# Performance work log

Measured on AMD Instinct MI355X. Metric: run time of the kernel, lower is better.

The kernel has to match this reference:

```python
import jax, jax.numpy as jnp
import numpy as np

EPS = 1e-5
K = 5


def _bn(h, g, b):
    # BatchNorm1d in training mode: batch stats over all dims except channels.
    ax = tuple(range(h.ndim - 1))
    mu = jnp.mean(h, axis=ax, keepdims=True)
    var = jnp.var(h, axis=ax, keepdims=True)
    return g * (h - mu) * jax.lax.rsqrt(var + EPS) + b


def _block(x, w, b, g, be):
    # Lin -> ReLU -> BN, as in MLP() helper
    return _bn(jax.nn.relu(x @ w + b), g, be)


def _knn_idx(x, k):
    # x: [B, P, D]; k nearest per point (includes self at distance 0)
    sq = jnp.sum(x * x, axis=-1)
    d2 = sq[:, :, None] + sq[:, None, :] - 2.0 * jnp.einsum('bpd,bqd->bpq', x, x)
    return jax.lax.top_k(-d2, k)[1]  # [B, P, k]


def _edge_conv(x, k, mlp_fn):
    # DynamicEdgeConv: recompute kNN graph on current features, gather
    # neighbor/center pairs, per-edge MLP on [x_i, x_j - x_i], max-aggregate.
    idx = _knn_idx(x, k)                                   # [B,P,k]
    xj = jax.vmap(lambda xb, ib: xb[ib])(x, idx)           # [B,P,k,D]
    xi = jnp.broadcast_to(x[:, :, None, :], xj.shape)
    e = jnp.concatenate([xi, xj - xi], axis=-1)            # [B,P,k,2D]
    return jnp.max(mlp_fn(e), axis=2)                      # max aggr -> [B,P,C]


def dec_forward(pos,
                c1w0, c1b0, c1g0, c1e0,
                c1w1, c1b1, c1g1, c1e1,
                c1w2, c1b2, c1g2, c1e2,
                c2w, c2b, c2g, c2e,
                l1w, l1b, l1g, l1e,
                m1w, m1b, m1g, m1e,
                m2w, m2b, m2g, m2e,
                m3w, m3b):
    mlp1 = lambda e: _block(_block(_block(e, c1w0, c1b0, c1g0, c1e0),
                                   c1w1, c1b1, c1g1, c1e1),
                            c1w2, c1b2, c1g2, c1e2)
    x1 = _edge_conv(pos, K, mlp1)                          # [B,P,64]
    x2 = _edge_conv(x1, K, lambda e: _block(e, c2w, c2b, c2g, c2e))  # [B,P,128]
    h = _block(jnp.concatenate([x1, x2], axis=-1), l1w, l1b, l1g, l1e)  # [B,P,1024]
    p = jnp.max(h, axis=1)                                 # global_max_pool -> [B,1024]
    p = _block(p, m1w, m1b, m1g, m1e)                      # dropout omitted (eval)
    p = _block(p, m2w, m2b, m2g, m2e)
    return p @ m3w + m3b                                   # [B, n_classes]


def setup_inputs() -> dict:
    key = jax.random.key(0)
    ks = jax.random.split(key, 12)
    B, P = 16, 2048

    def w(k, shape):
        return 0.05 * jax.random.normal(k, shape, jnp.float32)

    z = lambda c: jnp.zeros((c,), jnp.float32)
    o = lambda c: jnp.ones((c,), jnp.float32)

    d = {
        'pos': jax.random.normal(ks[0], (B, P, 3), jnp.float32),
        'c1w0': w(ks[1], (6, 64)), 'c1b0': z(64), 'c1g0': o(64), 'c1e0': z(64),
        'c1w1': w(ks[2], (64, 64)), 'c1b1': z(64), 'c1g1': o(64), 'c1e1': z(64),
        'c1w2': w(ks[3], (64, 64)), 'c1b2': z(64), 'c1g2': o(64), 'c1e2': z(64),
        'c2w': w(ks[4], (128, 128)), 'c2b': z(128), 'c2g': o(128), 'c2e': z(128),
        'l1w': w(ks[5], (192, 1024)), 'l1b': z(1024), 'l1g': o(1024), 'l1e': z(1024),
        'm1w': w(ks[6], (1024, 512)), 'm1b': z(512), 'm1g': o(512), 'm1e': z(512),
        'm2w': w(ks[7], (512, 256)), 'm2b': z(256), 'm2g': o(256), 'm2e': z(256),
        'm3w': w(ks[8], (256, 2)), 'm3b': z(2),
    }
    return d


def reference(pos,
              c1w0, c1b0, c1g0, c1e0,
              c1w1, c1b1, c1g1, c1e1,
              c1w2, c1b2, c1g2, c1e2,
              c2w, c2b, c2g, c2e,
              l1w, l1b, l1g, l1e,
              m1w, m1b, m1g, m1e,
              m2w, m2b, m2g, m2e,
              m3w, m3b):
    return dec_forward(pos,
                       c1w0, c1b0, c1g0, c1e0,
                       c1w1, c1b1, c1g1, c1e1,
                       c1w2, c1b2, c1g2, c1e2,
                       c2w, c2b, c2g, c2e,
                       l1w, l1b, l1g, l1e,
                       m1w, m1b, m1g, m1e,
                       m2w, m2b, m2g, m2e,
                       m3w, m3b)
```

## Files before the change

### kernel.cpp

```cpp
#include <hip/hip_runtime.h>
#include <cmath>

constexpr int B = 16, P = 2048, KNN = 5;
constexpr int BP = B * P;
constexpr int E = BP * KNN;
constexpr float EPS = 1e-5f;
constexpr int QC2 = 2;

constexpr int ST0 = 0;
constexpr int ST1 = 128;
constexpr int ST2 = 256;
constexpr int ST3 = 384;
constexpr int ST4 = 640;
constexpr int ST5 = 2688;
constexpr int ST6 = 3712;
constexpr int ST_TOTAL = 4224;

typedef __attribute__((ext_vector_type(8))) short bf16x8;
typedef __attribute__((ext_vector_type(4))) float f32x4;

__device__ inline unsigned short f2bf(float x) {
    unsigned u = __float_as_uint(x);
    unsigned r = (u + 0x7FFFu + ((u >> 16) & 1u)) >> 16;
    return (unsigned short)r;
}
__device__ inline float bf2f(unsigned short h) {
    return __uint_as_float(((unsigned)h) << 16);
}
__device__ inline void split2bf(float x, unsigned short& h, unsigned short& l) {
    unsigned short hh = f2bf(x);
    h = hh;
    l = f2bf(x - bf2f(hh));
}

__device__ inline void ins5(float d, int qi, float bd[KNN], int bi[KNN]) {
    bool c0 = d < bd[0], c1 = d < bd[1], c2 = d < bd[2], c3 = d < bd[3], c4 = d < bd[4];
    bd[4] = c3 ? bd[3] : (c4 ? d : bd[4]);  bi[4] = c3 ? bi[3] : (c4 ? qi : bi[4]);
    bd[3] = c2 ? bd[2] : (c3 ? d : bd[3]);  bi[3] = c2 ? bi[2] : (c3 ? qi : bi[3]);
    bd[2] = c1 ? bd[1] : (c2 ? d : bd[2]);  bi[2] = c1 ? bi[1] : (c2 ? qi : bi[2]);
    bd[1] = c0 ? bd[0] : (c1 ? d : bd[1]);  bi[1] = c0 ? bi[0] : (c1 ? qi : bi[1]);
    bd[0] = c0 ? d : bd[0];                 bi[0] = c0 ? qi : bi[0];
}
__device__ inline void ins5t(float d, int qi, float bd[KNN], int bi[KNN]) {
    bool c0 = (d < bd[0]) || (d == bd[0] && qi < bi[0]);
    bool c1 = (d < bd[1]) || (d == bd[1] && qi < bi[1]);
    bool c2 = (d < bd[2]) || (d == bd[2] && qi < bi[2]);
    bool c3 = (d < bd[3]) || (d == bd[3] && qi < bi[3]);
    bool c4 = (d < bd[4]) || (d == bd[4] && qi < bi[4]);
    bd[4] = c3 ? bd[3] : (c4 ? d : bd[4]);  bi[4] = c3 ? bi[3] : (c4 ? qi : bi[4]);
    bd[3] = c2 ? bd[2] : (c3 ? d : bd[3]);  bi[3] = c2 ? bi[2] : (c3 ? qi : bi[3]);
    bd[2] = c1 ? bd[1] : (c2 ? d : bd[2]);  bi[2] = c1 ? bi[1] : (c2 ? qi : bi[2]);
    bd[1] = c0 ? bd[0] : (c1 ? d : bd[1]);  bi[1] = c0 ? bi[0] : (c1 ? qi : bi[1]);
    bd[0] = c0 ? d : bd[0];                 bi[0] = c0 ? qi : bi[0];
}

__global__ void k_init(float* __restrict__ stats, float* __restrict__ pmax,
                       float* __restrict__ pmin) {
    int i = blockIdx.x * 256 + threadIdx.x;
    if (i < ST_TOTAL) stats[i] = 0.f;
    if (i < B * 1024) { pmax[i] = 0.f; pmin[i] = INFINITY; }
}

__global__ __launch_bounds__(256) void k_redstat(const float* __restrict__ part,
        float* __restrict__ stats, int nblk) {
    __shared__ float r[256];
    int slot = blockIdx.x;
    float s = 0.f;
    for (int i = threadIdx.x; i < nblk; i += 256)
        s += part[(size_t)i * 128 + slot];
    r[threadIdx.x] = s; __syncthreads();
    for (int o = 128; o; o >>= 1) {
        if (threadIdx.x < o) r[threadIdx.x] += r[threadIdx.x + o];
        __syncthreads();
    }
    if (threadIdx.x == 0) stats[slot] = r[0];
}

__global__ void k_wsplit(const float* __restrict__ w, unsigned short* __restrict__ th,
                         unsigned short* __restrict__ tl, int K, int N) {
    int i = blockIdx.x * 256 + threadIdx.x;
    if (i >= K * N) return;
    int k = i / N, n = i - k * N;
    float f = w[i];
    unsigned short h = f2bf(f);
    th[(size_t)n * K + k] = h;
    tl[(size_t)n * K + k] = f2bf(f - bf2f(h));
}

__global__ __launch_bounds__(64) void k_wfold(const float* __restrict__ stats,
        const float* __restrict__ g, const float* __restrict__ be,
        const float* __restrict__ w, const float* __restrict__ bias,
        unsigned short* __restrict__ wfh, unsigned short* __restrict__ wfl,
        float* __restrict__ bias2, float invN) {
    __shared__ float red[64];
    int n = blockIdx.x, k = threadIdx.x;
    float mu = stats[k] * invN;
    float var = stats[64 + k] * invN - mu * mu;
    float sc = g[k] * rsqrtf(var + EPS);
    float sh = be[k] - mu * sc;
    float wv = w[k * 64 + n];
    float wf = sc * wv;
    unsigned short h, l;
    split2bf(wf, h, l);
    wfh[n * 64 + k] = h; wfl[n * 64 + k] = l;
    red[k] = sh * wv; __syncthreads();
    for (int o = 32; o; o >>= 1) {
        if (k < o) red[k] += red[k + o];
        __syncthreads();
    }
    if (k == 0) bias2[n] = bias[n] + red[0];
}

__global__ void k_wprep2(const float* __restrict__ w,
        unsigned short* __restrict__ wdh, unsigned short* __restrict__ wdl,
        unsigned short* __restrict__ w1h, unsigned short* __restrict__ w1l) {
    int i = blockIdx.x * 256 + threadIdx.x;
    if (i >= 64 * 128) return;
    int k = i >> 7, n = i & 127;
    float w0 = w[k * 128 + n];
    float w1 = w[(64 + k) * 128 + n];
    float wd = w0 - w1;
    unsigned short h, l;
    split2bf(wd, h, l); wdh[n * 64 + k] = h; wdl[n * 64 + k] = l;
    split2bf(w1, h, l); w1h[n * 64 + k] = h; w1l[n * 64 + k] = l;
}

__global__ void k_xsplit(const float* __restrict__ x, unsigned short* __restrict__ xh,
                         unsigned short* __restrict__ xl) {
    int i = blockIdx.x * 256 + threadIdx.x;
    float f = x[i];
    unsigned short h, l;
    split2bf(f, h, l);
    xh[i] = h; xl[i] = l;
}

__global__ __launch_bounds__(256) void k_knn1(const float* __restrict__ pos,
                                              int* __restrict__ idx1) {
    __shared__ float4 qt[2048];
    int b = blockIdx.x >> 5;
    int p0 = (blockIdx.x & 31) << 6;
    const float* posb = pos + (size_t)b * P * 3;
#pragma unroll
    for (int t = 0; t < 8; ++t) {
        int q = (t << 8) + threadIdx.x;
        float qx = posb[q * 3 + 0], qy = posb[q * 3 + 1], qz = posb[q * 3 + 2];
        qt[q] = make_float4(qx, qy, qz, qx * qx + qy * qy + qz * qz);
    }
    __syncthreads();
    int pl = threadIdx.x >> 2, sub = threadIdx.x & 3;
    int p = p0 + pl;
    float4 me = qt[p];
    float x = me.x, y = me.y, z = me.z, sqp = me.w;
    float bd[KNN]; int bi[KNN];
#pragma unroll
    for (int i = 0; i < KNN; ++i) { bd[i] = INFINITY; bi[i] = 0; }
    for (int j0 = 0; j0 < 512; j0 += 8) {
        float4 v[8];
#pragma unroll
        for (int u = 0; u < 8; ++u) v[u] = qt[((j0 + u) << 2) | sub];
#pragma unroll
        for (int u = 0; u < 8; ++u) {
            float dot = x * v[u].x + y * v[u].y + z * v[u].z;
            float d2 = sqp + v[u].w - 2.f * dot;
            if (d2 < bd[KNN - 1]) ins5(d2, ((j0 + u) << 2) | sub, bd, bi);
        }
    }
#pragma unroll
    for (int w = 1; w <= 2; w <<= 1) {
        float od[KNN]; int oi[KNN];
#pragma unroll
        for (int i = 0; i < KNN; ++i) {
            od[i] = __shfl_xor(bd[i], w, 64);
            oi[i] = __shfl_xor(bi[i], w, 64);
        }
#pragma unroll
        for (int i = 0; i < KNN; ++i) ins5t(od[i], oi[i], bd, bi);
    }
    if (sub == 0) {
        size_t o = ((size_t)b * P + p) * KNN;
#pragma unroll
        for (int i = 0; i < KNN; ++i) idx1[o + i] = bi[i];
    }
}

__global__ __launch_bounds__(256) void k_ec1_l0(const float* __restrict__ pos,
        const int* __restrict__ idx1, const float* __restrict__ w,
        const float* __restrict__ bias, unsigned short* __restrict__ zh,
        unsigned short* __restrict__ zl, float* __restrict__ part) {
    __shared__ float elds[256][6];
    __shared__ float red[256];
    int tid = threadIdx.x;
    int base = blockIdx.x * 256;
    {
        int e = base + tid;
        int bp = e / KNN;
        int bb = bp >> 11;
        int q = idx1[e];
        const float* pi = pos + (size_t)bp * 3;
        const float* pj = pos + ((size_t)(bb << 11) + q) * 3;
        float x0 = pi[0], x1v = pi[1], x2v = pi[2];
        elds[tid][0] = x0; elds[tid][1] = x1v; elds[tid][2] = x2v;
        elds[tid][3] = pj[0] - x0; elds[tid][4] = pj[1] - x1v; elds[tid][5] = pj[2] - x2v;
    }
    int c = tid & 63, lane = tid >> 6;
    float wr[6];
#pragma unroll
    for (int d = 0; d < 6; ++d) wr[d] = w[d * 64 + c];
    float bc = bias[c];
    __syncthreads();
    float s1 = 0.f, s2 = 0.f;
    for (int i = 0; i < 64; ++i) {
        int e = lane + (i << 2);
        float acc = bc;
#pragma unroll
        for (int d = 0; d < 6; ++d) acc = fmaf(elds[e][d], wr[d], acc);
        acc = fmaxf(acc, 0.f);
        unsigned short h, l;
        split2bf(acc, h, l);
        zh[(size_t)(base + e) * 64 + c] = h;
        zl[(size_t)(base + e) * 64 + c] = l;
        s1 += acc; s2 = fmaf(acc, acc, s2);
    }
    red[tid] = s1; __syncthreads();
    if (tid < 64) part[(size_t)blockIdx.x * 128 + tid] =
        red[tid] + red[tid + 64] + red[tid + 128] + red[tid + 192];
    __syncthreads();
    red[tid] = s2; __syncthreads();
    if (tid < 64) part[(size_t)blockIdx.x * 128 + 64 + tid] =
        red[tid] + red[tid + 64] + red[tid + 128] + red[tid + 192];
}

__global__ __launch_bounds__(128) void k_lin64m(
        const unsigned short* __restrict__ zinh, const unsigned short* __restrict__ zinl,
        const unsigned short* __restrict__ wfh, const unsigned short* __restrict__ wfl,
        const float* __restrict__ bias2, unsigned short* __restrict__ zouth,
        unsigned short* __restrict__ zoutl, float* __restrict__ part) {
    __shared__ float red[2 * 64 * 2];
    int tid = threadIdx.x;
    int wv = tid >> 6, lane = tid & 63;
    int l15 = lane & 15, quad = lane >> 4;
    int row0 = blockIdx.x * 128 + wv * 64;
    f32x4 acc[4][4];
#pragma unroll
    for (int i = 0; i < 4; ++i)
#pragma unroll
        for (int j = 0; j < 4; ++j) acc[i][j] = (f32x4)0.f;

#pragma unroll
    for (int kc = 0; kc < 2; ++kc) {
        bf16x8 afh[4], afl[4], bfh[4], bfl[4];
#pragma unroll
        for (int i = 0; i < 4; ++i) {
            size_t o = (size_t)(row0 + i * 16 + l15) * 64 + kc * 32 + quad * 8;
            afh[i] = *(const bf16x8*)&zinh[o];
            afl[i] = *(const bf16x8*)&zinl[o];
        }
#pragma unroll
        for (int j = 0; j < 4; ++j) {
            size_t wo = (size_t)(j * 16 + l15) * 64 + kc * 32 + quad * 8;
            bfh[j] = *(const bf16x8*)&wfh[wo];
            bfl[j] = *(const bf16x8*)&wfl[wo];
        }
#pragma unroll
        for (int i = 0; i < 4; ++i)
#pragma unroll
            for (int j = 0; j < 4; ++j) {
                acc[i][j] = __builtin_amdgcn_mfma_f32_16x16x32_bf16(afh[i], bfh[j], acc[i][j], 0, 0, 0);
                acc[i][j] = __builtin_amdgcn_mfma_f32_16x16x32_bf16(afh[i], bfl[j], acc[i][j], 0, 0, 0);
                acc[i][j] = __builtin_amdgcn_mfma_f32_16x16x32_bf16(afl[i], bfh[j], acc[i][j], 0, 0, 0);
            }
    }
#pragma unroll
    for (int j = 0; j < 4; ++j) {
        int colL = j * 16 + l15;
        float bl = bias2[colL];
        float s1 = 0.f, s2 = 0.f;
#pragma unroll
        for (int i = 0; i < 4; ++i) {
            int row = row0 + i * 16 + quad * 4;
#pragma unroll
            for (int r = 0; r < 4; ++r) {
                float v = fmaxf(acc[i][j][r] + bl, 0.f);
                unsigned short h, l;
                split2bf(v, h, l);
                zouth[(size_t)(row + r) * 64 + colL] = h;
                zoutl[(size_t)(row + r) * 64 + colL] = l;
                s1 += v; s2 = fmaf(v, v, s2);
            }
        }
        s1 += __shfl_xor(s1, 16, 64); s1 += __shfl_xor(s1, 32, 64);
        s2 += __shfl_xor(s2, 16, 64); s2 += __shfl_xor(s2, 32, 64);
        if (quad == 0) {
            red[(wv * 64 + colL) * 2 + 0] = s1;
            red[(wv * 64 + colL) * 2 + 1] = s2;
        }
    }
    __syncthreads();
    if (tid < 64) {
        part[(size_t)blockIdx.x * 128 + tid] =
            red[tid * 2] + red[(64 + tid) * 2];
        part[(size_t)blockIdx.x * 128 + 64 + tid] =
            red[tid * 2 + 1] + red[(64 + tid) * 2 + 1];
    }
}

__global__ __launch_bounds__(256) void k_ec1_fin(const unsigned short* __restrict__ z2h,
        const unsigned short* __restrict__ z2l,
        const float* __restrict__ statsIn, const float* __restrict__ g,
        const float* __restrict__ be, float* __restrict__ x1,
        float* __restrict__ sq2) {
    int tid = threadIdx.x;
    int o = blockIdx.x * 256 + tid;
    int c = o & 63; int bp = o >> 6;
    float mu = statsIn[c] * (1.f / E);
    float var = statsIn[64 + c] * (1.f / E) - mu * mu;
    float sc = g[c] * rsqrtf(var + EPS);
    float sh = be[c] - mu * sc;
    float m = -INFINITY;
#pragma unroll
    for (int j = 0; j < KNN; ++j) {
        size_t zo = ((size_t)bp * KNN + j) * 64 + c;
        float v = bf2f(z2h[zo]) + bf2f(z2l[zo]);
        m = fmaxf(m, fmaf(v, sc, sh));
    }
    x1[o] = m;
    float ss = m * m;
#pragma unroll
    for (int off = 32; off; off >>= 1) ss += __shfl_down(ss, off, 64);
    if (c == 0) sq2[bp] = ss;
}

__global__ __launch_bounds__(128, 1) void k_knn2(const unsigned short* __restrict__ x1h,
        const unsigned short* __restrict__ x1l, const float* __restrict__ sq2,
        float* __restrict__ cd, int* __restrict__ ci) {
    __shared__ float S[2][32 * 129];
    int tid = threadIdx.x;
    int wv = tid >> 6, lane = tid & 63;
    int l15 = lane & 15, quad = lane >> 4;
    int qc = blockIdx.x & (QC2 - 1);
    int pt = blockIdx.x >> 1;
    int b = pt >> 5;
    int pw = ((pt & 31) << 6) + wv * 32;
    const size_t xbase = (size_t)b * P * 64;
    float* Sw = &S[wv][0];

    bf16x8 ah[2][2], al[2][2];
#pragma unroll
    for (int i = 0; i < 2; ++i)
#pragma unroll
        for (int kc = 0; kc < 2; ++kc) {
            size_t o = xbase + (size_t)(pw + i * 16 + l15) * 64 + kc * 32 + quad * 8;
            ah[i][kc] = *(const bf16x8*)&x1h[o];
            al[i][kc] = *(const bf16x8*)&x1l[o];
        }

    int half = lane >> 5;
    int pidx = lane & 31;
    float bd[KNN]; int bi[KNN];
#pragma unroll
    for (int i = 0; i < KNN; ++i) { bd[i] = INFINITY; bi[i] = 0; }

    int qlo = qc << 10;
    for (int t = 0; t < 8; ++t) {
        int q0 = qlo + (t << 7);
        float qsv[8];
#pragma unroll
        for (int j = 0; j < 8; ++j) qsv[j] = sq2[b * P + q0 + j * 16 + l15];
        f32x4 acc[2][8];
#pragma unroll
        for (int i = 0; i < 2; ++i)
#pragma unroll
            for (int j = 0; j < 8; ++j) acc[i][j] = (f32x4)0.f;
#pragma unroll
        for (int kc = 0; kc < 2; ++kc) {
            bf16x8 bh[8], bl[8];
#pragma unroll
            for (int j = 0; j < 8; ++j) {
                size_t o = xbase + (size_t)(q0 + j * 16 + l15) * 64 + kc * 32 + quad * 8;
                bh[j] = *(const bf16x8*)&x1h[o];
                bl[j] = *(const bf16x8*)&x1l[o];
            }
#pragma unroll
            for (int i = 0; i < 2; ++i)
#pragma unroll
                for (int j = 0; j < 8; ++j) {
                    acc[i][j] = __builtin_amdgcn_mfma_f32_16x16x32_bf16(ah[i][kc], bh[j], acc[i][j], 0, 0, 0);
                    acc[i][j] = __builtin_amdgcn_mfma_f32_16x16x32_bf16(ah[i][kc], bl[j], acc[i][j], 0, 0, 0);
                    acc[i][j] = __builtin_amdgcn_mfma_f32_16x16x32_bf16(al[i][kc], bh[j], acc[i][j], 0, 0, 0);
                }
        }
#pragma unroll
        for (int i = 0; i < 2; ++i)
#pragma unroll
            for (int j = 0; j < 8; ++j)
#pragma unroll
                for (int r = 0; r < 4; ++r) {
                    int pl = i * 16 + quad * 4 + r;
                    Sw[pl * 129 + j * 16 + l15] = fmaf(acc[i][j][r], -2.f, qsv[j]);
                }
        const float* row = Sw + pidx * 129 + half * 64;
        int qb = q0 + half * 64;
        for (int jj = 0; jj < 64; jj += 4) {
            float k0 = row[jj + 0], k1 = row[jj + 1], k2 = row[jj + 2], k3 = row[jj + 3];
            if (k0 < bd[4]) ins5(k0, qb + jj + 0, bd, bi);
            if (k1 < bd[4]) ins5(k1, qb + jj + 1, bd, bi);
            if (k2 < bd[4]) ins5(k2, qb + jj + 2, bd, bi);
            if (k3 < bd[4]) ins5(k3, qb + jj + 3, bd, bi);
        }
    }
#pragma unroll
    for (int i = 0; i < KNN; ++i) {
        float od = __shfl_xor(bd[i], 32, 64);
        int oi = __shfl_xor(bi[i], 32, 64);
        if (half == 0) ins5t(od, oi, bd, bi);
    }
    if (half == 0) {
        size_t o = (((size_t)b * P + pw + pidx) * QC2 + qc) * KNN;
#pragma unroll
        for (int i = 0; i < KNN; ++i) { cd[o + i] = bd[i]; ci[o + i] = bi[i]; }
    }
}

__global__ __launch_bounds__(256) void k_knn2m(const float* __restrict__ cd,
        const int* __restrict__ ci, int* __restrict__ idx2) {
    int bp = blockIdx.x * 256 + threadIdx.x;
    float bd[KNN]; int bi[KNN];
#pragma unroll
    for (int i = 0; i < KNN; ++i) { bd[i] = INFINITY; bi[i] = 0; }
    size_t o = (size_t)bp * QC2 * KNN;
    for (int t = 0; t < QC2 * KNN; ++t) {
        float d2 = cd[o + t]; int qi = ci[o + t];
        if (d2 < bd[KNN - 1]) ins5(d2, qi, bd, bi);
    }
#pragma unroll
    for (int i = 0; i < KNN; ++i) idx2[bp * KNN + i] = bi[i];
}

__global__ __launch_bounds__(256) void k_ec2m(
        const unsigned short* __restrict__ x1h, const unsigned short* __restrict__ x1l,
        const int* __restrict__ idx2,
        const unsigned short* __restrict__ wdh, const unsigned short* __restrict__ wdl,
        const unsigned short* __restrict__ w1h, const unsigned short* __restrict__ w1l,
        const float* __restrict__ bias, float* __restrict__ zout,
        float* __restrict__ stats) {
    __shared__ float red[2 * 128 * 2];
    int tid = threadIdx.x;
    int base = blockIdx.x * 128;
    int bb = base / (P * KNN);
    int wv = tid >> 6, lane = tid & 63;
    int wm = wv >> 1, wn = wv & 1;
    int l15 = lane & 15, quad = lane >> 4;
    int rI[4], rJ[4];
#pragma unroll
    for (int i = 0; i < 4; ++i) {
        int e = base + wm * 64 + i * 16 + l15;
        rI[i] = e / KNN;
        rJ[i] = (bb << 11) + idx2[e];
    }
    f32x4 acc[4][4];
#pragma unroll
    for (int i = 0; i < 4; ++i)
#pragma unroll
        for (int j = 0; j < 4; ++j) acc[i][j] = (f32x4)0.f;

#pragma unroll
    for (int s = 0; s < 2; ++s) {
        const unsigned short* bh_ = s ? w1h : wdh;
        const unsigned short* bl_ = s ? w1l : wdl;
#pragma unroll
        for (int kc = 0; kc < 2; ++kc) {
            bf16x8 afh[4], afl[4], bfh[4], bfl[4];
#pragma unroll
            for (int i = 0; i < 4; ++i) {
                int row = s ? rJ[i] : rI[i];
                size_t o = (size_t)row * 64 + kc * 32 + quad * 8;
                afh[i] = *(const bf16x8*)&x1h[o];
                afl[i] = *(const bf16x8*)&x1l[o];
            }
#pragma unroll
            for (int j = 0; j < 4; ++j) {
                size_t wo = (size_t)(wn * 64 + j * 16 + l15) * 64 + kc * 32 + quad * 8;
                bfh[j] = *(const bf16x8*)&bh_[wo];
                bfl[j] = *(const bf16x8*)&bl_[wo];
            }
#pragma unroll
            for (int i = 0; i < 4; ++i)
#pragma unroll
                for (int j = 0; j < 4; ++j) {
                    acc[i][j] = __builtin_amdgcn_mfma_f32_16x16x32_bf16(afh[i], bfh[j], acc[i][j], 0, 0, 0);
                    acc[i][j] = __builtin_amdgcn_mfma_f32_16x16x32_bf16(afh[i], bfl[j], acc[i][j], 0, 0, 0);
                    acc[i][j] = __builtin_amdgcn_mfma_f32_16x16x32_bf16(afl[i], bfh[j], acc[i][j], 0, 0, 0);
                }
        }
    }
#pragma unroll
    for (int j = 0; j < 4; ++j) {
        int colL = wn * 64 + j * 16 + l15;
        float bl = bias[colL];
        float s1 = 0.f, s2 = 0.f;
#pragma unroll
        for (int i = 0; i < 4; ++i) {
            int row = wm * 64 + i * 16 + quad * 4;
#pragma unroll
            for (int r = 0; r < 4; ++r) {
                float v = fmaxf(acc[i][j][r] + bl, 0.f);
                zout[(size_t)(base + row + r) * 128 + colL] = v;
                s1 += v; s2 = fmaf(v, v, s2);
            }
        }
        s1 += __shfl_xor(s1, 16, 64); s1 += __shfl_xor(s1, 32, 64);
        s2 += __shfl_xor(s2, 16, 64); s2 += __shfl_xor(s2, 32, 64);
        if (quad == 0) {
            red[(wm * 128 + colL) * 2 + 0] = s1;
            red[(wm * 128 + colL) * 2 + 1] = s2;
        }
    }
    __syncthreads();
    if (tid < 128) {
        atomicAdd(&stats[tid], red[tid * 2] + red[(128 + tid) * 2]);
        atomicAdd(&stats[128 + tid], red[tid * 2 + 1] + red[(128 + tid) * 2 + 1]);
    }
}

__global__ __launch_bounds__(256) void k_ec2_fin(const float* __restrict__ z3,
        const float* __restrict__ stats, const float* __restrict__ g,
        const float* __restrict__ be, float* __restrict__ x2) {
    int o = blockIdx.x * 256 + threadIdx.x;
    int c = o & 127; int bp = o >> 7;
    float mu = stats[c] * (1.f / E);
    float var = stats[128 + c] * (1.f / E) - mu * mu;
    float sc = g[c] * rsqrtf(var + EPS);
    float sh = be[c] - mu * sc;
    float m = -INFINITY;
#pragma unroll
    for (int j = 0; j < KNN; ++j)
        m = fmaxf(m, fmaf(z3[((size_t)bp * KNN + j) * 128 + c], sc, sh));
    x2[o] = m;
}

__global__ __launch_bounds__(256) void k_l1m(
        const unsigned short* __restrict__ x1h, const unsigned short* __restrict__ x1l,
        const unsigned short* __restrict__ x2h, const unsigned short* __restrict__ x2l,
        const unsigned short* __restrict__ wth, const unsigned short* __restrict__ wtl,
        const float* __restrict__ bias, float* __restrict__ stats,
        float* __restrict__ pmax, float* __restrict__ pmin) {
    __shared__ float red[2 * 128 * 4];
    int tid = threadIdx.x;
    int brow = blockIdx.x & 255;
    int bcol = blockIdx.x >> 8;
    int row0 = brow << 7, col0 = bcol << 7;
    int wv = tid >> 6, lane = tid & 63;
    int wm = wv >> 1, wn = wv & 1;
    int l15 = lane & 15, quad = lane >> 4;
    f32x4 acc[4][4];
#pragma unroll
    for (int i = 0; i < 4; ++i)
#pragma unroll
        for (int j = 0; j < 4; ++j) acc[i][j] = (f32x4)0.f;

    auto loadA = [&](int k0, bf16x8* fh, bf16x8* fl) {
        const unsigned short* ah = (k0 < 64) ? x1h : x2h;
        const unsigned short* al = (k0 < 64) ? x1l : x2l;
        int astr = (k0 < 64) ? 64 : 128;
        int aoff = (k0 < 64) ? k0 : (k0 - 64);
#pragma unroll
        for (int i = 0; i < 4; ++i) {
            size_t o = (size_t)(row0 + wm * 64 + i * 16 + l15) * astr + aoff + quad * 8;
            fh[i] = *(const bf16x8*)&ah[o];
            fl[i] = *(const bf16x8*)&al[o];
        }
    };
    auto loadB = [&](int k0, bf16x8* fh, bf16x8* fl) {
#pragma unroll
        for (int j = 0; j < 4; ++j) {
            size_t wo = (size_t)(col0 + wn * 64 + j * 16 + l15) * 192 + k0 + quad * 8;
            fh[j] = *(const bf16x8*)&wth[wo];
            fl[j] = *(const bf16x8*)&wtl[wo];
        }
    };
    auto compute = [&](bf16x8* afh, bf16x8* afl, bf16x8* bfh, bf16x8* bfl) {
#pragma unroll
        for (int i = 0; i < 4; ++i)
#pragma unroll
            for (int j = 0; j < 4; ++j) {
                acc[i][j] = __builtin_amdgcn_mfma_f32_16x16x32_bf16(afh[i], bfh[j], acc[i][j], 0, 0, 0);
                acc[i][j] = __builtin_amdgcn_mfma_f32_16x16x32_bf16(afh[i], bfl[j], acc[i][j], 0, 0, 0);
                acc[i][j] = __builtin_amdgcn_mfma_f32_16x16x32_bf16(afl[i], bfh[j], acc[i][j], 0, 0, 0);
            }
    };

    bf16x8 A0h[4], A0l[4], B0h[4], B0l[4];
    bf16x8 A1h[4], A1l[4], B1h[4], B1l[4];
    loadA(0, A0h, A0l); loadB(0, B0h, B0l);
#pragma unroll
    for (int t = 0; t < 6; ++t) {
        if ((t & 1) == 0) {
            if (t < 5) { loadA((t + 1) * 32, A1h, A1l); loadB((t + 1) * 32, B1h, B1l); }
            compute(A0h, A0l, B0h, B0l);
        } else {
            if (t < 5) { loadA((t + 1) * 32, A0h, A0l); loadB((t + 1) * 32, B0h, B0l); }
            compute(A1h, A1l, B1h, B1l);
        }
    }
#pragma unroll
    for (int j = 0; j < 4; ++j) {
        int colL = wn * 64 + j * 16 + l15;
        float bl = bias[col0 + colL];
        float s1 = 0.f, s2 = 0.f, mx = 0.f, mn = INFINITY;
#pragma unroll
        for (int i = 0; i < 4; ++i)
#pragma unroll
            for (int r = 0; r < 4; ++r) {
                float v = fmaxf(acc[i][j][r] + bl, 0.f);
                s1 += v; s2 = fmaf(v, v, s2);
                mx = fmaxf(mx, v); mn = fminf(mn, v);
            }
        s1 += __shfl_xor(s1, 16, 64); s1 += __shfl_xor(s1, 32, 64);
        s2 += __shfl_xor(s2, 16, 64); s2 += __shfl_xor(s2, 32, 64);
        mx = fmaxf(mx, __shfl_xor(mx, 16, 64)); mx = fmaxf(mx, __shfl_xor(mx, 32, 64));
        mn = fminf(mn, __shfl_xor(mn, 16, 64)); mn = fminf(mn, __shfl_xor(mn, 32, 64));
        if (quad == 0) {
            float* rp = &red[(wm * 128 + colL) * 4];
            rp[0] = s1; rp[1] = s2; rp[2] = mx; rp[3] = mn;
        }
    }
    __syncthreads();
    if (tid < 128) {
        const float* r0 = &red[tid * 4];
        const float* r1 = &red[(128 + tid) * 4];
        int bb = row0 >> 11;
        atomicAdd(&stats[col0 + tid], r0[0] + r1[0]);
        atomicAdd(&stats[1024 + col0 + tid], r0[1] + r1[1]);
        atomicMax((unsigned int*)&pmax[bb * 1024 + col0 + tid],
                  __float_as_uint(fmaxf(r0[2], r1[2])));
        atomicMin((unsigned int*)&pmin[bb * 1024 + col0 + tid],
                  __float_as_uint(fminf(r0[3], r1[3])));
    }
}

__global__ void k_pool(const float* __restrict__ stats, const float* __restrict__ g,
                       const float* __restrict__ be, const float* __restrict__ pmax,
                       const float* __restrict__ pmin, float* __restrict__ p) {
    int o = blockIdx.x * 256 + threadIdx.x;
    int c = o & 1023;
    float mu = stats[c] * (1.f / BP);
    float var = stats[1024 + c] * (1.f / BP) - mu * mu;
    float sc = g[c] * rsqrtf(var + EPS);
    float sh = be[c] - mu * sc;
    float v = (sc >= 0.f) ? pmax[o] : pmin[o];
    p[o] = fmaf(v, sc, sh);
}

__global__ __launch_bounds__(256) void k_m1(const float* __restrict__ p,
        const float* __restrict__ w, const float* __restrict__ bias,
        float* __restrict__ t1, float* __restrict__ stats) {
    int o = blockIdx.x * 256 + threadIdx.x;
    int c = o & 511, b = o >> 9;
    const float* pr = p + (b << 10);
    float acc = bias[c];
    for (int k = 0; k < 1024; ++k) acc = fmaf(pr[k], w[k * 512 + c], acc);
    acc = fmaxf(acc, 0.f);
    t1[o] = acc;
    atomicAdd(&stats[c], acc);
    atomicAdd(&stats[512 + c], acc * acc);
}

__global__ __launch_bounds__(256) void k_m2(const float* __restrict__ t1,
        const float* __restrict__ stats5, const float* __restrict__ g,
        const float* __restrict__ be, const float* __restrict__ w,
        const float* __restrict__ bias, float* __restrict__ t2,
        float* __restrict__ stats6) {
    __shared__ float scl[512], shf[512];
    int tid = threadIdx.x;
    for (int t = tid; t < 512; t += 256) {
        float mu = stats5[t] * (1.f / 16.f);
        float var = stats5[512 + t] * (1.f / 16.f) - mu * mu;
        float sc = g[t] * rsqrtf(var + EPS);
        scl[t] = sc; shf[t] = be[t] - mu * sc;
    }
    __syncthreads();
    int o = blockIdx.x * 256 + tid;
    int c = o & 255, b = o >> 8;
    const float* tr = t1 + (b << 9);
    float acc = bias[c];
    for (int k = 0; k < 512; ++k) {
        float u = fmaf(tr[k], scl[k], shf[k]);
        acc = fmaf(u, w[k * 256 + c], acc);
    }
    acc = fmaxf(acc, 0.f);
    t2[o] = acc;
    atomicAdd(&stats6[c], acc);
    atomicAdd(&stats6[256 + c], acc * acc);
}

__global__ __launch_bounds__(256) void k_m3(const float* __restrict__ t2,
        const float* __restrict__ stats6, const float* __restrict__ g,
        const float* __restrict__ be, const float* __restrict__ w,
        const float* __restrict__ bias, float* __restrict__ out) {
    __shared__ float scl[256], shf[256];
    int tid = threadIdx.x;
    {
        float mu = stats6[tid] * (1.f / 16.f);
        float var = stats6[256 + tid] * (1.f / 16.f) - mu * mu;
        float sc = g[tid] * rsqrtf(var + EPS);
        scl[tid] = sc; shf[tid] = be[tid] - mu * sc;
    }
    __syncthreads();
    if (tid < 32) {
        int c = tid & 1, b = tid >> 1;
        const float* tr = t2 + (b << 8);
        float acc = bias[c];
        for (int k = 0; k < 256; ++k) {
            float u = fmaf(tr[k], scl[k], shf[k]);
            acc = fmaf(u, w[k * 2 + c], acc);
        }
        out[tid] = acc;
    }
}

extern "C" void kernel_launch(void* const* d_in, const int* in_sizes, int n_in,
                              void* d_out, int out_size, void* d_ws, size_t ws_size,
                              hipStream_t stream) {
    const float* pos  = (const float*)d_in[0];
    const float* c1w0 = (const float*)d_in[1];
    const float* c1b0 = (const float*)d_in[2];
    const float* c1g0 = (const float*)d_in[3];
    const float* c1e0 = (const float*)d_in[4];
    const float* c1w1 = (const float*)d_in[5];
    const float* c1b1 = (const float*)d_in[6];
    const float* c1g1 = (const float*)d_in[7];
    const float* c1e1 = (const float*)d_in[8];
    const float* c1w2 = (const float*)d_in[9];
    const float* c1b2 = (const float*)d_in[10];
    const float* c1g2 = (const float*)d_in[11];
    const float* c1e2 = (const float*)d_in[12];
    const float* c2w  = (const float*)d_in[13];
    const float* c2b  = (const float*)d_in[14];
    const float* c2g  = (const float*)d_in[15];
    const float* c2e  = (const float*)d_in[16];
    const float* l1w  = (const float*)d_in[17];
    const float* l1b  = (const float*)d_in[18];
    const float* l1g  = (const float*)d_in[19];
    const float* l1e  = (const float*)d_in[20];
    const float* m1w  = (const float*)d_in[21];
    const float* m1b  = (const float*)d_in[22];
    const float* m1g  = (const float*)d_in[23];
    const float* m1e  = (const float*)d_in[24];
    const float* m2w  = (const float*)d_in[25];
    const float* m2b  = (const float*)d_in[26];
    const float* m2g  = (const float*)d_in[27];
    const float* m2e  = (const float*)d_in[28];
    const float* m3w  = (const float*)d_in[29];
    const float* m3b  = (const float*)d_in[30];
    float* out = (float*)d_out;

    char* ws = (char*)d_ws;
    size_t off = 0;
    auto alloc = [&](size_t bytes) {
        size_t r = off; off = (off + bytes + 255) & ~(size_t)255; return r;
    };
    float* stats = (float*)(ws + alloc(ST_TOTAL * 4));
    float* pmax  = (float*)(ws + alloc(16 * 1024 * 4));
    float* pmin  = (float*)(ws + alloc(16 * 1024 * 4));
    float* pbuf  = (float*)(ws + alloc(16 * 1024 * 4));
    float* t1    = (float*)(ws + alloc(16 * 512 * 4));
    float* t2    = (float*)(ws + alloc(16 * 256 * 4));
    float* sq2   = (float*)(ws + alloc((size_t)BP * 4));
    float* part  = (float*)(ws + alloc((size_t)(E / 64) * 128 * 4));
    unsigned short* wthL = (unsigned short*)(ws + alloc((size_t)192 * 1024 * 2));
    unsigned short* wtlL = (unsigned short*)(ws + alloc((size_t)192 * 1024 * 2));
    unsigned short* wdh  = (unsigned short*)(ws + alloc((size_t)128 * 64 * 2));
    unsigned short* wdl  = (unsigned short*)(ws + alloc((size_t)128 * 64 * 2));
    unsigned short* w1h  = (unsigned short*)(ws + alloc((size_t)128 * 64 * 2));
    unsigned short* w1l  = (unsigned short*)(ws + alloc((size_t)128 * 64 * 2));
    unsigned short* wf1h = (unsigned short*)(ws + alloc((size_t)64 * 64 * 2));
    unsigned short* wf1l = (unsigned short*)(ws + alloc((size_t)64 * 64 * 2));
    unsigned short* wf2h = (unsigned short*)(ws + alloc((size_t)64 * 64 * 2));
    unsigned short* wf2l = (unsigned short*)(ws + alloc((size_t)64 * 64 * 2));
    float* bias2a = (float*)(ws + alloc(64 * 4));
    float* bias2b = (float*)(ws + alloc(64 * 4));
    int*   idx1  = (int*)  (ws + alloc((size_t)E * 4));
    int*   idx2  = (int*)  (ws + alloc((size_t)E * 4));
    float* x1    = (float*)(ws + alloc((size_t)BP * 64 * 4));
    float* x2    = (float*)(ws + alloc((size_t)BP * 128 * 4));
    float* zA    = (float*)(ws + alloc((size_t)E * 128 * 4));
    float* zB    = (float*)(ws + alloc((size_t)E * 64 * 4));
    unsigned short* z0h = (unsigned short*)zA;
    unsigned short* z0l = z0h + (size_t)E * 64;
    unsigned short* z1h = z0l + (size_t)E * 64;
    unsigned short* z1l = z1h + (size_t)E * 64;
    unsigned short* z2h = (unsigned short*)zB;
    unsigned short* z2l = z2h + (size_t)E * 64;
    unsigned short* x1h = (unsigned short*)zB;
    unsigned short* x1l = x1h + (size_t)BP * 64;
    float* cand_d = (float*)(x1l + (size_t)BP * 64);
    int*   cand_i = (int*)(cand_d + (size_t)BP * QC2 * KNN);
    unsigned short* x2h = (unsigned short*)(cand_i + (size_t)BP * QC2 * KNN);
    unsigned short* x2l = x2h + (size_t)BP * 128;

    (void)in_sizes; (void)n_in; (void)out_size; (void)ws_size;

    k_init<<<64, 256, 0, stream>>>(stats, pmax, pmin);
    k_wsplit<<<(192 * 1024 + 255) / 256, 256, 0, stream>>>(l1w, wthL, wtlL, 192, 1024);
    k_wprep2<<<(64 * 128 + 255) / 256, 256, 0, stream>>>(c2w, wdh, wdl, w1h, w1l);
    k_knn1<<<B * 32, 256, 0, stream>>>(pos, idx1);
    k_ec1_l0<<<E / 256, 256, 0, stream>>>(pos, idx1, c1w0, c1b0, z0h, z0l, part);
    k_redstat<<<128, 256, 0, stream>>>(part, stats + ST0, E / 256);
    k_wfold<<<64, 64, 0, stream>>>(stats + ST0, c1g0, c1e0, c1w1, c1b1,
                                   wf1h, wf1l, bias2a, 1.f / E);
    k_lin64m<<<E / 128, 128, 0, stream>>>(z0h, z0l, wf1h, wf1l, bias2a,
                                          z1h, z1l, part);
    k_redstat<<<128, 256, 0, stream>>>(part, stats + ST1, E / 128);
    k_wfold<<<64, 64, 0, stream>>>(stats + ST1, c1g1, c1e1, c1w2, c1b2,
                                   wf2h, wf2l, bias2b, 1.f / E);
    k_lin64m<<<E / 128, 128, 0, stream>>>(z1h, z1l, wf2h, wf2l, bias2b,
                                          z2h, z2l, part);
    k_redstat<<<128, 256, 0, stream>>>(part, stats + ST2, E / 128);
    k_ec1_fin<<<BP * 64 / 256, 256, 0, stream>>>(z2h, z2l, stats + ST2, c1g2, c1e2,
                                                 x1, sq2);
    k_xsplit<<<BP * 64 / 256, 256, 0, stream>>>(x1, x1h, x1l);
    k_knn2<<<B * 32 * QC2, 128, 0, stream>>>(x1h, x1l, sq2, cand_d, cand_i);
    k_knn2m<<<BP / 256, 256, 0, stream>>>(cand_d, cand_i, idx2);
    k_ec2m<<<E / 128, 256, 0, stream>>>(x1h, x1l, idx2, wdh, wdl, w1h, w1l,
                                        c2b, zA, stats + ST3);
    k_ec2_fin<<<BP * 128 / 256, 256, 0, stream>>>(zA, stats + ST3, c2g, c2e, x2);
    k_xsplit<<<BP * 128 / 256, 256, 0, stream>>>(x2, x2h, x2l);
    k_l1m<<<256 * 8, 256, 0, stream>>>(x1h, x1l, x2h, x2l, wthL, wtlL, l1b,
                                       stats + ST4, pmax, pmin);
    k_pool<<<64, 256, 0, stream>>>(stats + ST4, l1g, l1e, pmax, pmin, pbuf);
    k_m1<<<32, 256, 0, stream>>>(pbuf, m1w, m1b, t1, stats + ST5);
    k_m2<<<16, 256, 0, stream>>>(t1, stats + ST5, m1g, m1e, m2w, m2b, t2, stats + ST6);
    k_m3<<<1, 256, 0, stream>>>(t2, stats + ST6, m2g, m2e, m3w, m3b, out);
}
```

Baseline: 629.4 us.

## Stage l1 GEMM tiles through LDS with direct global-to-LDS loads

The k_l1m GEMM kernel used to load A and B fragments straight from global memory into registers, with a double-buffered register prefetch. It now copies each 32-wide K slice of the hi/lo A and B tiles into shared memory using global_load_lds, then reads the MFMA fragments from LDS. Each element is fetched from global once per block instead of once per wave, which cuts redundant traffic and register pressure. The cost is that register prefetch overlap is gone: there are two barriers per K step and only one LDS buffer, so load latency is exposed.

Measured after the change: 586.6 us. 6.8% less time.

```diff
diff --git a/kernel.cpp b/kernel.cpp
--- a/kernel.cpp
+++ b/kernel.cpp
@@ -538,12 +538,20 @@
     x2[o] = m;
 }
 
+__device__ __forceinline__ void gl16(unsigned short* lds, const unsigned short* g) {
+    __builtin_amdgcn_global_load_lds(
+        (const __attribute__((address_space(1))) unsigned int*)g,
+        (__attribute__((address_space(3))) unsigned int*)lds, 16, 0, 0);
+}
+
 __global__ __launch_bounds__(256) void k_l1m(
         const unsigned short* __restrict__ x1h, const unsigned short* __restrict__ x1l,
         const unsigned short* __restrict__ x2h, const unsigned short* __restrict__ x2l,
         const unsigned short* __restrict__ wth, const unsigned short* __restrict__ wtl,
         const float* __restrict__ bias, float* __restrict__ stats,
         float* __restrict__ pmax, float* __restrict__ pmin) {
+    __shared__ unsigned short Ah[128 * 32], Al[128 * 32];
+    __shared__ unsigned short Bh[128 * 32], Bl[128 * 32];
     __shared__ float red[2 * 128 * 4];
     int tid = threadIdx.x;
     int brow = blockIdx.x & 255;
@@ -552,33 +560,46 @@
     int wv = tid >> 6, lane = tid & 63;
     int wm = wv >> 1, wn = wv & 1;
     int l15 = lane & 15, quad = lane >> 4;
+    int rloc = wv * 16 + (lane >> 2);
+    int ch8 = (lane & 3) * 8;
     f32x4 acc[4][4];
 #pragma unroll
     for (int i = 0; i < 4; ++i)
 #pragma unroll
         for (int j = 0; j < 4; ++j) acc[i][j] = (f32x4)0.f;
 
-    auto loadA = [&](int k0, bf16x8* fh, bf16x8* fl) {
+#pragma unroll
+    for (int t = 0; t < 6; ++t) {
+        int k0 = t * 32;
         const unsigned short* ah = (k0 < 64) ? x1h : x2h;
         const unsigned short* al = (k0 < 64) ? x1l : x2l;
         int astr = (k0 < 64) ? 64 : 128;
         int aoff = (k0 < 64) ? k0 : (k0 - 64);
 #pragma unroll
+        for (int c = 0; c < 2; ++c) {
+            int rl = c * 64 + rloc;
+            size_t ao = (size_t)(row0 + rl) * astr + aoff + ch8;
+            size_t bo = (size_t)(col0 + rl) * 192 + k0 + ch8;
+            int lb = (c * 64 + wv * 16) * 32;
+            gl16(&Ah[lb], &ah[ao]);
+            gl16(&Al[lb], &al[ao]);
+            gl16(&Bh[lb], &wth[bo]);
+            gl16(&Bl[lb], &wtl[bo]);
+        }
+        __syncthreads();
+        bf16x8 afh[4], afl[4], bfh[4], bfl[4];
+#pragma unroll
         for (int i = 0; i < 4; ++i) {
-            size_t o = (size_t)(row0 + wm * 64 + i * 16 + l15) * astr + aoff + quad * 8;
-            fh[i] = *(const bf16x8*)&ah[o];
-            fl[i] = *(const bf16x8*)&al[o];
-        }
-    };
-    auto loadB = [&](int k0, bf16x8* fh, bf16x8* fl) {
+            int o = (wm * 64 + i * 16 + l15) * 32 + quad * 8;
+            afh[i] = *(const bf16x8*)&Ah[o];
+            afl[i] = *(const bf16x8*)&Al[o];
+        }
 #pragma unroll
         for (int j = 0; j < 4; ++j) {
-            size_t wo = (size_t)(col0 + wn * 64 + j * 16 + l15) * 192 + k0 + quad * 8;
-            fh[j] = *(const bf16x8*)&wth[wo];
-            fl[j] = *(const bf16x8*)&wtl[wo];
-        }
-    };
-    auto compute = [&](bf16x8* afh, bf16x8* afl, bf16x8* bfh, bf16x8* bfl) {
+            int o = (wn * 64 + j * 16 + l15) * 32 + quad * 8;
+            bfh[j] = *(const bf16x8*)&Bh[o];
+            bfl[j] = *(const bf16x8*)&Bl[o];
+        }
 #pragma unroll
         for (int i = 0; i < 4; ++i)
 #pragma unroll
@@ -587,20 +608,7 @@
                 acc[i][j] = __builtin_amdgcn_mfma_f32_16x16x32_bf16(afh[i], bfl[j], acc[i][j], 0, 0, 0);
                 acc[i][j] = __builtin_amdgcn_mfma_f32_16x16x32_bf16(afl[i], bfh[j], acc[i][j], 0, 0, 0);
             }
-    };
-
-    bf16x8 A0h[4], A0l[4], B0h[4], B0l[4];
-    bf16x8 A1h[4], A1l[4], B1h[4], B1l[4];
-    loadA(0, A0h, A0l); loadB(0, B0h, B0l);
-#pragma unroll
-    for (int t = 0; t < 6; ++t) {
-        if ((t & 1) == 0) {
-            if (t < 5) { loadA((t + 1) * 32, A1h, A1l); loadB((t + 1) * 32, B1h, B1l); }
-            compute(A0h, A0l, B0h, B0l);
-        } else {
-            if (t < 5) { loadA((t + 1) * 32, A0h, A0l); loadB((t + 1) * 32, B0h, B0l); }
-            compute(A1h, A1l, B1h, B1l);
-        }
+        __syncthreads();
     }
 #pragma unroll
     for (int j = 0; j < 4; ++j) {
```
